# Kernel tuning notes

Measured on AMD Instinct MI355X. Metric: run time of the kernel, lower is better.

Reference implementation:

```python
import jax, jax.numpy as jnp
import numpy as np

C_IN = 1.0
C_OUT = 1.0
N_NODES = 10000
D_IN = 256
D_OUT = 256
N_EDGES = 320000
MIN_NORM = 1e-15
BALL_EPS = 4e-3  # float32 boundary eps used by HGCN PoincareBall


def _norm(x):
    return jnp.maximum(jnp.linalg.norm(x, axis=-1, keepdims=True), MIN_NORM)


def _artanh(x):
    x = jnp.clip(x, -1.0 + 1e-7, 1.0 - 1e-7)
    return 0.5 * (jnp.log1p(x) - jnp.log1p(-x))


def proj(x, c):
    norm = _norm(x)
    maxnorm = (1.0 - BALL_EPS) / jnp.sqrt(c)
    return jnp.where(norm > maxnorm, x / norm * maxnorm, x)


def expmap0(u, c):
    sc = jnp.sqrt(c)
    un = _norm(u)
    return jnp.tanh(sc * un) * u / (sc * un)


def logmap0(p, c):
    sc = jnp.sqrt(c)
    pn = _norm(p)
    return _artanh(sc * pn) * p / (sc * pn)


def mobius_add(x, y, c):
    x2 = jnp.sum(x * x, -1, keepdims=True)
    y2 = jnp.sum(y * y, -1, keepdims=True)
    xy = jnp.sum(x * y, -1, keepdims=True)
    num = (1 + 2 * c * xy + c * y2) * x + (1 - c * x2) * y
    denom = 1 + 2 * c * xy + c * c * x2 * y2
    return num / jnp.maximum(denom, MIN_NORM)


def mobius_matvec(m, x, c):
    sc = jnp.sqrt(c)
    xn = _norm(x)
    mx = x @ m.T  # [N, D_out]
    mxn = _norm(mx)
    res = jnp.tanh(mxn / xn * _artanh(sc * xn)) * mx / (mxn * sc)
    cond = jnp.all(mx == 0, axis=-1, keepdims=True)
    return jnp.where(cond, jnp.zeros_like(res), res)


def setup_inputs() -> dict:
    key = jax.random.key(0)
    k = jax.random.split(key, 6)
    x = jax.random.normal(k[0], (N_NODES, D_IN), jnp.float32) * 0.05
    x = proj(x, C_IN)  # valid points on the Poincare ball
    weight = jax.random.normal(k[1], (D_OUT, D_IN), jnp.float32) * (1.0 / np.sqrt(D_IN))
    bias = jax.random.normal(k[2], (D_OUT,), jnp.float32) * 0.01
    adj_val = jax.random.uniform(k[3], (N_EDGES,), jnp.float32) * (1.0 / 32.0)
    adj_row = jnp.sort(jax.random.randint(k[4], (N_EDGES,), 0, N_NODES, jnp.int32))
    adj_col = jax.random.randint(k[5], (N_EDGES,), 0, N_NODES, jnp.int32)
    return {"x": x, "weight": weight, "bias": bias, "adj_val": adj_val,
            "adj_row": adj_row, "adj_col": adj_col}


def reference(x, weight, bias, adj_val, adj_row, adj_col):
    # --- HypLinear: mobius matvec + hyperbolic bias ---
    h = proj(mobius_matvec(weight, x, C_IN), C_IN)
    hyp_bias = proj(expmap0(bias[None, :], C_IN), C_IN)  # proj_tan0 is identity
    h = proj(mobius_add(h, hyp_bias, C_IN), C_IN)
    # --- HypAgg: tangent-space sparse aggregation ---
    x_t = logmap0(h, C_IN)  # [N, D_out]
    msgs = adj_val[:, None] * x_t[adj_col]  # [E, D_out]
    support_t = jax.ops.segment_sum(msgs, adj_row, num_segments=N_NODES)
    h = proj(expmap0(support_t, C_IN), C_IN)
    # --- HypAct: act in tangent space, remap with c_out ---
    xt = jax.nn.relu(logmap0(h, C_IN))
    return proj(expmap0(xt, C_OUT), C_OUT)
```

## Files before the change

kernel.cpp:

```cpp
#include <hip/hip_runtime.h>
#include <math.h>

#define D 256
#define MAXNORM (1.0f - 4e-3f)
#define MIN_NORM 1e-15f

typedef _Float16 v8h __attribute__((ext_vector_type(8)));
typedef _Float16 h4  __attribute__((ext_vector_type(4)));
typedef float    v4f __attribute__((ext_vector_type(4)));

__device__ __forceinline__ float wave_reduce_sum(float v) {
    #pragma unroll
    for (int m = 32; m >= 1; m >>= 1) v += __shfl_xor(v, m, 64);
    return v;
}

__device__ __forceinline__ float dot4(const float4& a, const float4& b) {
    return a.x * b.x + a.y * b.y + a.z * b.z + a.w * b.w;
}

__device__ __forceinline__ float artanh_clip(float x) {
    x = fminf(fmaxf(x, -1.0f + 1e-7f), 1.0f - 1e-7f);
    return 0.5f * (log1pf(x) - log1pf(-x));
}

__global__ void bias_kernel(const float* __restrict__ bias, float* __restrict__ hb) {
    int l = threadIdx.x;
    float4 v = *(const float4*)(bias + 4 * l);
    float bn = fmaxf(sqrtf(wave_reduce_sum(dot4(v, v))), MIN_NORM);
    float f = tanhf(bn) / bn;
    float4 h = make_float4(v.x * f, v.y * f, v.z * f, v.w * f);
    float hn = fmaxf(sqrtf(wave_reduce_sum(dot4(h, h))), MIN_NORM);
    float s = (hn > MAXNORM) ? (MAXNORM / hn) : 1.0f;
    h.x *= s; h.y *= s; h.z *= s; h.w *= s;
    *(float4*)(hb + 4 * l) = h;
    float y2 = wave_reduce_sum(dot4(h, h));
    if (l == 0) hb[D] = y2;
}

__global__ __launch_bounds__(256) void rowptr_kernel(
    const int* __restrict__ rows, int* __restrict__ rowptr, int N, int E)
{
    int e = blockIdx.x * blockDim.x + threadIdx.x;
    if (e >= E) return;
    int r1 = rows[e];
    if (e == 0) {
        for (int r = 0; r <= r1; ++r) rowptr[r] = 0;
    } else {
        int r0 = rows[e - 1];
        for (int r = r0 + 1; r <= r1; ++r) rowptr[r] = e;
    }
    if (e == E - 1) {
        for (int r = r1 + 1; r <= N; ++r) rowptr[r] = E;
    }
}

__global__ __launch_bounds__(256) void wcast_kernel(
    const float* __restrict__ W, _Float16* __restrict__ Wh)
{
    int i = blockIdx.x * blockDim.x + threadIdx.x;
    float4 v = ((const float4*)W)[i];
    h4 o; o[0] = (_Float16)v.x; o[1] = (_Float16)v.y;
    o[2] = (_Float16)v.z; o[3] = (_Float16)v.w;
    *(h4*)(Wh + 4 * (size_t)i) = o;
}

#define AS_STRIDE 264

__global__ __launch_bounds__(256) void gemm_kernel(
    const float* __restrict__ X, const _Float16* __restrict__ Wh,
    float* __restrict__ MX, float* __restrict__ XNSQ, int N)
{
    __shared__ _Float16 As[32 * AS_STRIDE];
    const int t = threadIdx.x;
    const int r0 = blockIdx.x * 32;

    {
        const int r = t >> 3;
        const int q = t & 7;
        const int grow = r0 + r;
        float ss = 0.0f;
        #pragma unroll
        for (int j = 0; j < 8; ++j) {
            const int fi = q + j * 8;
            float4 v = make_float4(0.f, 0.f, 0.f, 0.f);
            if (grow < N) v = ((const float4*)X)[(size_t)grow * 64 + fi];
            ss += dot4(v, v);
            h4 hv; hv[0] = (_Float16)v.x; hv[1] = (_Float16)v.y;
            hv[2] = (_Float16)v.z; hv[3] = (_Float16)v.w;
            *(h4*)&As[r * AS_STRIDE + fi * 4] = hv;
        }
        ss += __shfl_xor(ss, 1, 64);
        ss += __shfl_xor(ss, 2, 64);
        ss += __shfl_xor(ss, 4, 64);
        if (q == 0 && grow < N) XNSQ[grow] = ss;
    }
    __syncthreads();

    const int w  = t >> 6;
    const int l  = t & 63;
    const int lm = l & 15;
    const int q  = l >> 4;

    v4f acc[2][4];
    #pragma unroll
    for (int a = 0; a < 2; ++a)
        #pragma unroll
        for (int b = 0; b < 4; ++b)
            #pragma unroll
            for (int i = 0; i < 4; ++i) acc[a][b][i] = 0.0f;

    const _Float16* WhB = Wh + (size_t)(64 * w + lm) * 256 + q * 8;

    #pragma unroll
    for (int kc = 0; kc < 8; ++kc) {
        const int k = kc * 32 + q * 8;
        v8h a0 = *(const v8h*)&As[(0  + lm) * AS_STRIDE + k];
        v8h a1 = *(const v8h*)&As[(16 + lm) * AS_STRIDE + k];
        #pragma unroll
        for (int ct = 0; ct < 4; ++ct) {
            v8h b = *(const v8h*)(WhB + (size_t)ct * 16 * 256 + kc * 32);
            acc[0][ct] = __builtin_amdgcn_mfma_f32_16x16x32_f16(a0, b, acc[0][ct], 0, 0, 0);
            acc[1][ct] = __builtin_amdgcn_mfma_f32_16x16x32_f16(a1, b, acc[1][ct], 0, 0, 0);
        }
    }

    #pragma unroll
    for (int rt = 0; rt < 2; ++rt)
        #pragma unroll
        for (int ct = 0; ct < 4; ++ct)
            #pragma unroll
            for (int i = 0; i < 4; ++i) {
                const int row = r0 + rt * 16 + q * 4 + i;
                if (row < N)
                    MX[(size_t)row * 256 + 64 * w + ct * 16 + lm] = acc[rt][ct][i];
            }
}

__global__ __launch_bounds__(256) void rowops_kernel(
    const float* __restrict__ MX, const float* __restrict__ XNSQ,
    const float* __restrict__ HB, _Float16* __restrict__ XT, int N)
{
    int wave = (int)((blockIdx.x * (size_t)blockDim.x + threadIdx.x) >> 6);
    int l = threadIdx.x & 63;
    if (wave >= N) return;

    const float4 mxv = *(const float4*)(MX + (size_t)wave * D + 4 * l);
    float xn  = fmaxf(sqrtf(XNSQ[wave]), MIN_NORM);
    float mxn = fmaxf(sqrtf(wave_reduce_sum(dot4(mxv, mxv))), MIN_NORM);

    float r = (mxn / xn) * artanh_clip(xn);
    float f = tanhf(r) / mxn;
    float4 h = make_float4(mxv.x * f, mxv.y * f, mxv.z * f, mxv.w * f);

    float hss = wave_reduce_sum(dot4(h, h));
    float hn = fmaxf(sqrtf(hss), MIN_NORM);
    float s = (hn > MAXNORM) ? (MAXNORM / hn) : 1.0f;
    h.x *= s; h.y *= s; h.z *= s; h.w *= s;
    float x2 = hss * s * s;

    const float4 y = *(const float4*)(HB + 4 * l);
    float y2 = HB[D];
    float xy = wave_reduce_sum(dot4(h, y));
    float ch = 1.0f + 2.0f * xy + y2;
    float cy = 1.0f - x2;
    float den = fmaxf(1.0f + 2.0f * xy + x2 * y2, MIN_NORM);
    float inv = 1.0f / den;
    float4 g = make_float4((ch * h.x + cy * y.x) * inv,
                           (ch * h.y + cy * y.y) * inv,
                           (ch * h.z + cy * y.z) * inv,
                           (ch * h.w + cy * y.w) * inv);

    float gss = wave_reduce_sum(dot4(g, g));
    float gn = fmaxf(sqrtf(gss), MIN_NORM);
    float s2 = (gn > MAXNORM) ? (MAXNORM / gn) : 1.0f;
    g.x *= s2; g.y *= s2; g.z *= s2; g.w *= s2;

    float pn = fmaxf(gn * s2, MIN_NORM);
    float lf = artanh_clip(pn) / pn;
    h4 xt; xt[0] = (_Float16)(g.x * lf); xt[1] = (_Float16)(g.y * lf);
    xt[2] = (_Float16)(g.z * lf); xt[3] = (_Float16)(g.w * lf);
    *(h4*)(XT + (size_t)wave * D + 4 * l) = xt;
}

__global__ __launch_bounds__(256) void agg_kernel(
    const int* __restrict__ rowptr, const int* __restrict__ cols,
    const float* __restrict__ vals, const _Float16* __restrict__ XT,
    float* __restrict__ OUT, int N)
{
    int node = (int)((blockIdx.x * (size_t)blockDim.x + threadIdx.x) >> 6);
    int l = threadIdx.x & 63;
    if (node >= N) return;

    int start = rowptr[node];
    int end   = rowptr[node + 1];

    const h4* xt4 = (const h4*)XT;
    float4 acc = make_float4(0.f, 0.f, 0.f, 0.f);

    for (int base = start; base < end; base += 64) {
        int idx = base + l;
        bool ok = idx < end;
        int   myc = ok ? cols[idx] : 0;
        float myv = ok ? vals[idx] : 0.0f;
        int cnt = min(64, end - base);
        int cnt8 = (cnt + 7) & ~7;

        for (int j = 0; j < cnt8; j += 8) {
            int   c[8];
            float v[8];
            #pragma unroll
            for (int u = 0; u < 8; ++u) {
                c[u] = __shfl(myc, j + u, 64);
                v[u] = __shfl(myv, j + u, 64);
            }
            h4 m[8];
            #pragma unroll
            for (int u = 0; u < 8; ++u)
                m[u] = xt4[(size_t)c[u] * 64 + l];
            #pragma unroll
            for (int u = 0; u < 8; ++u) {
                acc.x = fmaf(v[u], (float)m[u][0], acc.x);
                acc.y = fmaf(v[u], (float)m[u][1], acc.y);
                acc.z = fmaf(v[u], (float)m[u][2], acc.z);
                acc.w = fmaf(v[u], (float)m[u][3], acc.w);
            }
        }
    }

    float un = fmaxf(sqrtf(wave_reduce_sum(dot4(acc, acc))), MIN_NORM);
    float f = tanhf(un) / un;
    float4 h = make_float4(acc.x * f, acc.y * f, acc.z * f, acc.w * f);
    float hn = fmaxf(sqrtf(wave_reduce_sum(dot4(h, h))), MIN_NORM);
    float s = (hn > MAXNORM) ? (MAXNORM / hn) : 1.0f;
    h.x *= s; h.y *= s; h.z *= s; h.w *= s;
    float pn = fmaxf(hn * s, MIN_NORM);
    float lf = artanh_clip(pn) / pn;
    float4 tt = make_float4(fmaxf(h.x * lf, 0.f), fmaxf(h.y * lf, 0.f),
                            fmaxf(h.z * lf, 0.f), fmaxf(h.w * lf, 0.f));
    float un2 = fmaxf(sqrtf(wave_reduce_sum(dot4(tt, tt))), MIN_NORM);
    float f2 = tanhf(un2) / un2;
    float4 o = make_float4(tt.x * f2, tt.y * f2, tt.z * f2, tt.w * f2);
    float on = fmaxf(sqrtf(wave_reduce_sum(dot4(o, o))), MIN_NORM);
    float s2 = (on > MAXNORM) ? (MAXNORM / on) : 1.0f;
    o.x *= s2; o.y *= s2; o.z *= s2; o.w *= s2;

    *(float4*)(OUT + (size_t)node * D + 4 * l) = o;
}

extern "C" void kernel_launch(void* const* d_in, const int* in_sizes, int n_in,
                              void* d_out, int out_size, void* d_ws, size_t ws_size,
                              hipStream_t stream) {
    const float* X    = (const float*)d_in[0];
    const float* W    = (const float*)d_in[1];
    const float* bias = (const float*)d_in[2];
    const float* vals = (const float*)d_in[3];
    const int*   rows = (const int*)d_in[4];
    const int*   cols = (const int*)d_in[5];
    float* OUT = (float*)d_out;

    const int N = in_sizes[0] / D;
    const int E = in_sizes[3];

    int*   rowptr = (int*)d_ws;
    float* HB   = (float*)d_ws + 10240;
    float* XNSQ = HB + 512;
    _Float16* Wh = (_Float16*)(XNSQ + 10240);
    _Float16* XT = (_Float16*)((float*)(void*)Wh + 16384 + 64);
    float* MX = OUT;

    bias_kernel<<<1, 64, 0, stream>>>(bias, HB);
    rowptr_kernel<<<(E + 255) / 256, 256, 0, stream>>>(rows, rowptr, N, E);
    wcast_kernel<<<64, 256, 0, stream>>>(W, Wh);
    gemm_kernel<<<(N + 31) / 32, 256, 0, stream>>>(X, Wh, MX, XNSQ, N);
    int wave_blocks = (N + 3) / 4;
    rowops_kernel<<<wave_blocks, 256, 0, stream>>>(MX, XNSQ, HB, XT, N);
    agg_kernel<<<wave_blocks, 256, 0, stream>>>(rowptr, cols, vals, XT, OUT, N);
}
```

Measured before the change: 122.7 us.

## Fuse prep kernels and fold row-wise hyperbolic ops into GEMM epilogue

Merges the bias, rowptr and weight-cast kernels into one prep kernel, which saves launches. The per-row mobius/proj/logmap math moves into the GEMM epilogue, so the fp32 MX intermediate no longer takes a global round trip. The row norms and dot products with the bias are reduced from the MFMA accumulators through shared memory, and each row's output becomes A*mx + B*y. The GEMM tile shrinks to 16 rows per block, which lowers the MFMA work per block and drops the reuse of the weight loads across two row tiles.

```diff
diff --git a/kernel.cpp b/kernel.cpp
--- a/kernel.cpp
+++ b/kernel.cpp
@@ -24,76 +24,85 @@
     return 0.5f * (log1pf(x) - log1pf(-x));
 }
 
-__global__ void bias_kernel(const float* __restrict__ bias, float* __restrict__ hb) {
-    int l = threadIdx.x;
-    float4 v = *(const float4*)(bias + 4 * l);
-    float bn = fmaxf(sqrtf(wave_reduce_sum(dot4(v, v))), MIN_NORM);
-    float f = tanhf(bn) / bn;
-    float4 h = make_float4(v.x * f, v.y * f, v.z * f, v.w * f);
-    float hn = fmaxf(sqrtf(wave_reduce_sum(dot4(h, h))), MIN_NORM);
-    float s = (hn > MAXNORM) ? (MAXNORM / hn) : 1.0f;
-    h.x *= s; h.y *= s; h.z *= s; h.w *= s;
-    *(float4*)(hb + 4 * l) = h;
-    float y2 = wave_reduce_sum(dot4(h, h));
-    if (l == 0) hb[D] = y2;
-}
-
-__global__ __launch_bounds__(256) void rowptr_kernel(
-    const int* __restrict__ rows, int* __restrict__ rowptr, int N, int E)
+__global__ __launch_bounds__(256) void prep_kernel(
+    const float* __restrict__ bias, const float* __restrict__ W,
+    const int* __restrict__ rows,
+    float* __restrict__ HB, _Float16* __restrict__ Wh,
+    int* __restrict__ rowptr, int N, int E)
 {
-    int e = blockIdx.x * blockDim.x + threadIdx.x;
-    if (e >= E) return;
-    int r1 = rows[e];
-    if (e == 0) {
-        for (int r = 0; r <= r1; ++r) rowptr[r] = 0;
-    } else {
-        int r0 = rows[e - 1];
-        for (int r = r0 + 1; r <= r1; ++r) rowptr[r] = e;
-    }
-    if (e == E - 1) {
-        for (int r = r1 + 1; r <= N; ++r) rowptr[r] = E;
-    }
-}
-
-__global__ __launch_bounds__(256) void wcast_kernel(
-    const float* __restrict__ W, _Float16* __restrict__ Wh)
+    const int b = blockIdx.x, t = threadIdx.x;
+    const int e = b * 256 + t;
+
+    if (e < E) {
+        int r1 = rows[e];
+        if (e == 0) {
+            for (int r = 0; r <= r1; ++r) rowptr[r] = 0;
+        } else {
+            int r0 = rows[e - 1];
+            for (int r = r0 + 1; r <= r1; ++r) rowptr[r] = e;
+        }
+        if (e == E - 1) {
+            for (int r = r1 + 1; r <= N; ++r) rowptr[r] = E;
+        }
+    }
+
+    if (b < 64) {
+        int i = b * 256 + t;
+        float4 v = ((const float4*)W)[i];
+        h4 o; o[0] = (_Float16)v.x; o[1] = (_Float16)v.y;
+        o[2] = (_Float16)v.z; o[3] = (_Float16)v.w;
+        *(h4*)(Wh + 4 * (size_t)i) = o;
+    }
+
+    if (b == 64 && t < 64) {
+        int l = t;
+        float4 v = *(const float4*)(bias + 4 * l);
+        float bn = fmaxf(sqrtf(wave_reduce_sum(dot4(v, v))), MIN_NORM);
+        float f = tanhf(bn) / bn;
+        float4 h = make_float4(v.x * f, v.y * f, v.z * f, v.w * f);
+        float hn = fmaxf(sqrtf(wave_reduce_sum(dot4(h, h))), MIN_NORM);
+        float s = (hn > MAXNORM) ? (MAXNORM / hn) : 1.0f;
+        h.x *= s; h.y *= s; h.z *= s; h.w *= s;
+        *(float4*)(HB + 4 * l) = h;
+        float y2 = wave_reduce_sum(dot4(h, h));
+        if (l == 0) HB[D] = y2;
+    }
+}
+
+#define AS16 264
+
+__global__ __launch_bounds__(256) void gemmrow_kernel(
+    const float* __restrict__ X, const _Float16* __restrict__ Wh,
+    const float* __restrict__ HB, _Float16* __restrict__ XT, int N)
 {
-    int i = blockIdx.x * blockDim.x + threadIdx.x;
-    float4 v = ((const float4*)W)[i];
-    h4 o; o[0] = (_Float16)v.x; o[1] = (_Float16)v.y;
-    o[2] = (_Float16)v.z; o[3] = (_Float16)v.w;
-    *(h4*)(Wh + 4 * (size_t)i) = o;
-}
-
-#define AS_STRIDE 264
-
-__global__ __launch_bounds__(256) void gemm_kernel(
-    const float* __restrict__ X, const _Float16* __restrict__ Wh,
-    float* __restrict__ MX, float* __restrict__ XNSQ, int N)
-{
-    __shared__ _Float16 As[32 * AS_STRIDE];
+    __shared__ _Float16 As[16 * AS16];
+    __shared__ float xnsq[16];
+    __shared__ float part_s[16][4];
+    __shared__ float part_d[16][4];
+    __shared__ float Arow[16], Brow[16];
+
     const int t = threadIdx.x;
-    const int r0 = blockIdx.x * 32;
+    const int r0 = blockIdx.x * 16;
 
     {
-        const int r = t >> 3;
-        const int q = t & 7;
+        const int r = t >> 4, q2 = t & 15;
         const int grow = r0 + r;
         float ss = 0.0f;
         #pragma unroll
-        for (int j = 0; j < 8; ++j) {
-            const int fi = q + j * 8;
+        for (int j = 0; j < 4; ++j) {
+            const int fi = q2 + j * 16;
             float4 v = make_float4(0.f, 0.f, 0.f, 0.f);
             if (grow < N) v = ((const float4*)X)[(size_t)grow * 64 + fi];
             ss += dot4(v, v);
             h4 hv; hv[0] = (_Float16)v.x; hv[1] = (_Float16)v.y;
             hv[2] = (_Float16)v.z; hv[3] = (_Float16)v.w;
-            *(h4*)&As[r * AS_STRIDE + fi * 4] = hv;
+            *(h4*)&As[r * AS16 + fi * 4] = hv;
         }
         ss += __shfl_xor(ss, 1, 64);
         ss += __shfl_xor(ss, 2, 64);
         ss += __shfl_xor(ss, 4, 64);
-        if (q == 0 && grow < N) XNSQ[grow] = ss;
+        ss += __shfl_xor(ss, 8, 64);
+        if (q2 == 0) xnsq[r] = ss;
     }
     __syncthreads();
 
@@ -102,85 +111,98 @@
     const int lm = l & 15;
     const int q  = l >> 4;
 
-    v4f acc[2][4];
-    #pragma unroll
-    for (int a = 0; a < 2; ++a)
-        #pragma unroll
-        for (int b = 0; b < 4; ++b)
-            #pragma unroll
-            for (int i = 0; i < 4; ++i) acc[a][b][i] = 0.0f;
+    v4f acc[4];
+    #pragma unroll
+    for (int ct = 0; ct < 4; ++ct)
+        #pragma unroll
+        for (int i = 0; i < 4; ++i) acc[ct][i] = 0.0f;
 
     const _Float16* WhB = Wh + (size_t)(64 * w + lm) * 256 + q * 8;
 
     #pragma unroll
     for (int kc = 0; kc < 8; ++kc) {
-        const int k = kc * 32 + q * 8;
-        v8h a0 = *(const v8h*)&As[(0  + lm) * AS_STRIDE + k];
-        v8h a1 = *(const v8h*)&As[(16 + lm) * AS_STRIDE + k];
+        v8h a = *(const v8h*)&As[lm * AS16 + kc * 32 + q * 8];
         #pragma unroll
         for (int ct = 0; ct < 4; ++ct) {
-            v8h b = *(const v8h*)(WhB + (size_t)ct * 16 * 256 + kc * 32);
-            acc[0][ct] = __builtin_amdgcn_mfma_f32_16x16x32_f16(a0, b, acc[0][ct], 0, 0, 0);
-            acc[1][ct] = __builtin_amdgcn_mfma_f32_16x16x32_f16(a1, b, acc[1][ct], 0, 0, 0);
-        }
-    }
-
-    #pragma unroll
-    for (int rt = 0; rt < 2; ++rt)
-        #pragma unroll
-        for (int ct = 0; ct < 4; ++ct)
+            v8h bfr = *(const v8h*)(WhB + (size_t)ct * 16 * 256 + kc * 32);
+            acc[ct] = __builtin_amdgcn_mfma_f32_16x16x32_f16(a, bfr, acc[ct], 0, 0, 0);
+        }
+    }
+
+    float yv[4];
+    #pragma unroll
+    for (int ct = 0; ct < 4; ++ct) yv[ct] = HB[64 * w + ct * 16 + lm];
+
+    {
+        float s_[4], d_[4];
+        #pragma unroll
+        for (int i = 0; i < 4; ++i) {
+            float s = 0.f, d = 0.f;
+            #pragma unroll
+            for (int ct = 0; ct < 4; ++ct) {
+                float v = acc[ct][i];
+                s = fmaf(v, v, s);
+                d = fmaf(v, yv[ct], d);
+            }
+            #pragma unroll
+            for (int m = 1; m <= 8; m <<= 1) {
+                s += __shfl_xor(s, m, 64);
+                d += __shfl_xor(d, m, 64);
+            }
+            s_[i] = s; d_[i] = d;
+        }
+        if (lm == 0) {
             #pragma unroll
             for (int i = 0; i < 4; ++i) {
-                const int row = r0 + rt * 16 + q * 4 + i;
-                if (row < N)
-                    MX[(size_t)row * 256 + 64 * w + ct * 16 + lm] = acc[rt][ct][i];
-            }
-}
-
-__global__ __launch_bounds__(256) void rowops_kernel(
-    const float* __restrict__ MX, const float* __restrict__ XNSQ,
-    const float* __restrict__ HB, _Float16* __restrict__ XT, int N)
-{
-    int wave = (int)((blockIdx.x * (size_t)blockDim.x + threadIdx.x) >> 6);
-    int l = threadIdx.x & 63;
-    if (wave >= N) return;
-
-    const float4 mxv = *(const float4*)(MX + (size_t)wave * D + 4 * l);
-    float xn  = fmaxf(sqrtf(XNSQ[wave]), MIN_NORM);
-    float mxn = fmaxf(sqrtf(wave_reduce_sum(dot4(mxv, mxv))), MIN_NORM);
-
-    float r = (mxn / xn) * artanh_clip(xn);
-    float f = tanhf(r) / mxn;
-    float4 h = make_float4(mxv.x * f, mxv.y * f, mxv.z * f, mxv.w * f);
-
-    float hss = wave_reduce_sum(dot4(h, h));
-    float hn = fmaxf(sqrtf(hss), MIN_NORM);
-    float s = (hn > MAXNORM) ? (MAXNORM / hn) : 1.0f;
-    h.x *= s; h.y *= s; h.z *= s; h.w *= s;
-    float x2 = hss * s * s;
-
-    const float4 y = *(const float4*)(HB + 4 * l);
-    float y2 = HB[D];
-    float xy = wave_reduce_sum(dot4(h, y));
-    float ch = 1.0f + 2.0f * xy + y2;
-    float cy = 1.0f - x2;
-    float den = fmaxf(1.0f + 2.0f * xy + x2 * y2, MIN_NORM);
-    float inv = 1.0f / den;
-    float4 g = make_float4((ch * h.x + cy * y.x) * inv,
-                           (ch * h.y + cy * y.y) * inv,
-                           (ch * h.z + cy * y.z) * inv,
-                           (ch * h.w + cy * y.w) * inv);
-
-    float gss = wave_reduce_sum(dot4(g, g));
-    float gn = fmaxf(sqrtf(gss), MIN_NORM);
-    float s2 = (gn > MAXNORM) ? (MAXNORM / gn) : 1.0f;
-    g.x *= s2; g.y *= s2; g.z *= s2; g.w *= s2;
-
-    float pn = fmaxf(gn * s2, MIN_NORM);
-    float lf = artanh_clip(pn) / pn;
-    h4 xt; xt[0] = (_Float16)(g.x * lf); xt[1] = (_Float16)(g.y * lf);
-    xt[2] = (_Float16)(g.z * lf); xt[3] = (_Float16)(g.w * lf);
-    *(h4*)(XT + (size_t)wave * D + 4 * l) = xt;
+                part_s[q * 4 + i][w] = s_[i];
+                part_d[q * 4 + i][w] = d_[i];
+            }
+        }
+    }
+    __syncthreads();
+
+    if (t < 16) {
+        float mx2 = part_s[t][0] + part_s[t][1] + part_s[t][2] + part_s[t][3];
+        float mxy = part_d[t][0] + part_d[t][1] + part_d[t][2] + part_d[t][3];
+        float y2  = HB[D];
+        float xn  = fmaxf(sqrtf(xnsq[t]), MIN_NORM);
+        float mxn = fmaxf(sqrtf(mx2), MIN_NORM);
+        float r  = (mxn / xn) * artanh_clip(xn);
+        float th = tanhf(r);
+        float f  = th / mxn;
+        float hn = fmaxf(th, MIN_NORM);
+        float s  = (hn > MAXNORM) ? (MAXNORM / hn) : 1.0f;
+        float fs = f * s;
+        float x2 = th * th * s * s;
+        float xy  = fs * mxy;
+        float ch  = 1.0f + 2.0f * xy + y2;
+        float cy  = 1.0f - x2;
+        float inv = 1.0f / fmaxf(1.0f + 2.0f * xy + x2 * y2, MIN_NORM);
+        float alpha = ch * fs * inv;
+        float beta  = cy * inv;
+        float gss = alpha * alpha * mx2 + 2.0f * alpha * beta * mxy + beta * beta * y2;
+        float gn  = fmaxf(sqrtf(gss), MIN_NORM);
+        float s2  = (gn > MAXNORM) ? (MAXNORM / gn) : 1.0f;
+        float pn  = fmaxf(gn * s2, MIN_NORM);
+        float lf  = artanh_clip(pn) / pn;
+        Arow[t] = lf * s2 * alpha;
+        Brow[t] = lf * s2 * beta;
+    }
+    __syncthreads();
+
+    #pragma unroll
+    for (int i = 0; i < 4; ++i) {
+        const int rr = q * 4 + i;
+        const int row = r0 + rr;
+        if (row < N) {
+            float A = Arow[rr], B = Brow[rr];
+            #pragma unroll
+            for (int ct = 0; ct < 4; ++ct) {
+                float v = fmaf(A, acc[ct][i], B * yv[ct]);
+                XT[(size_t)row * 256 + 64 * w + ct * 16 + lm] = (_Float16)v;
+            }
+        }
+    }
 }
 
 __global__ __launch_bounds__(256) void agg_kernel(
@@ -262,18 +284,13 @@
     const int N = in_sizes[0] / D;
     const int E = in_sizes[3];
 
-    int*   rowptr = (int*)d_ws;
-    float* HB   = (float*)d_ws + 10240;
-    float* XNSQ = HB + 512;
-    _Float16* Wh = (_Float16*)(XNSQ + 10240);
-    _Float16* XT = (_Float16*)((float*)(void*)Wh + 16384 + 64);
-    float* MX = OUT;
-
-    bias_kernel<<<1, 64, 0, stream>>>(bias, HB);
-    rowptr_kernel<<<(E + 255) / 256, 256, 0, stream>>>(rows, rowptr, N, E);
-    wcast_kernel<<<64, 256, 0, stream>>>(W, Wh);
-    gemm_kernel<<<(N + 31) / 32, 256, 0, stream>>>(X, Wh, MX, XNSQ, N);
+    int*      rowptr = (int*)d_ws;
+    float*    HB = (float*)d_ws + 10240;
+    _Float16* Wh = (_Float16*)((float*)d_ws + 10240 + 512);
+    _Float16* XT = (_Float16*)((float*)d_ws + 10240 + 512 + 32768);
+
+    prep_kernel<<<(E + 255) / 256, 256, 0, stream>>>(bias, W, rows, HB, Wh, rowptr, N, E);
+    gemmrow_kernel<<<(N + 15) / 16, 256, 0, stream>>>(X, Wh, HB, XT, N);
     int wave_blocks = (N + 3) / 4;
-    rowops_kernel<<<wave_blocks, 256, 0, stream>>>(MX, XNSQ, HB, XT, N);
     agg_kernel<<<wave_blocks, 256, 0, stream>>>(rowptr, cols, vals, XT, OUT, N);
 }
```

New measurement: 110.6 us. 1.11x faster.
